# Performance work log

Measured on AMD Instinct MI355X. Metric: run time of the kernel, lower is better.

The kernel has to match this reference:

```python
import jax, jax.numpy as jnp
import numpy as np

MODEL = 2048
LATENT = 512
POS = 1024
NH = 16
HD = MODEL // NH        # 128
PHD = POS // NH         # 64
THETA = 50000.0


def _rope_tables(S, dim, base=THETA):
    inv_freq = 1.0 / (base ** (jnp.arange(0, dim, 2, dtype=jnp.float32) / dim))
    t = jnp.arange(S, dtype=jnp.float32)
    freqs = jnp.outer(t, inv_freq)                  # [S, dim/2]
    emb = jnp.concatenate([freqs, freqs], axis=-1)  # [S, dim]
    return jnp.cos(emb), jnp.sin(emb)


def _rotate_half(x):
    h = x.shape[-1] // 2
    return jnp.concatenate([-x[..., h:], x[..., :h]], axis=-1)


def _apply_rope(x, cos, sin):
    # x: [..., S, dim]; cos/sin: [S, dim]
    return x * cos + _rotate_half(x) * sin


def setup_inputs() -> dict:
    key = jax.random.key(0)
    ks = jax.random.split(key, 16)
    std = 0.02
    d = {
        'x':      jax.random.normal(ks[0], (2, 2048, MODEL), jnp.float32),
        'w_qkv':  jax.random.normal(ks[1], (MODEL, 3 * LATENT), jnp.float32) * std,
        'b_qkv':  jnp.zeros((3 * LATENT,), jnp.float32),
        'w_qup':  jax.random.normal(ks[2], (LATENT, MODEL), jnp.float32) * std,
        'b_qup':  jnp.zeros((MODEL,), jnp.float32),
        'w_kup':  jax.random.normal(ks[3], (LATENT, MODEL), jnp.float32) * std,
        'b_kup':  jnp.zeros((MODEL,), jnp.float32),
        'w_vup':  jax.random.normal(ks[4], (LATENT, MODEL), jnp.float32) * std,
        'b_vup':  jnp.zeros((MODEL,), jnp.float32),
        'w_qpos': jax.random.normal(ks[5], (LATENT, POS), jnp.float32) * std,
        'b_qpos': jnp.zeros((POS,), jnp.float32),
        'w_kpos': jax.random.normal(ks[6], (MODEL, PHD), jnp.float32) * std,
        'b_kpos': jnp.zeros((PHD,), jnp.float32),
        'w_o':    jax.random.normal(ks[7], (MODEL, MODEL), jnp.float32) * std,
        'b_o':    jnp.zeros((MODEL,), jnp.float32),
    }
    return d


def reference(x, w_qkv, b_qkv, w_qup, b_qup, w_kup, b_kup, w_vup, b_vup,
              w_qpos, b_qpos, w_kpos, b_kpos, w_o, b_o):
    B, S, _ = x.shape
    # fused down-projection into shared latent
    latent_qkv = x @ w_qkv + b_qkv                       # [B,S,3L]
    lq, lk, lv = jnp.split(latent_qkv, 3, axis=-1)       # each [B,S,L]

    cos, sin = _rope_tables(S, PHD)

    # decoupled positional key (shared across heads), RoPE on sub-slice
    pos_k = x @ w_kpos + b_kpos                          # [B,S,PHD]
    pos_k = _apply_rope(pos_k, cos, sin)

    # up-projections
    q = (lq @ w_qup + b_qup).reshape(B, S, NH, HD).transpose(0, 2, 1, 3)
    k = (lk @ w_kup + b_kup).reshape(B, S, NH, HD).transpose(0, 2, 1, 3)
    v = (lv @ w_vup + b_vup).reshape(B, S, NH, HD).transpose(0, 2, 1, 3)

    pos_q = (lq @ w_qpos + b_qpos).reshape(B, S, NH, PHD).transpose(0, 2, 1, 3)
    pos_q = _apply_rope(pos_q, cos, sin)                 # [B,NH,S,PHD]

    pos_kh = jnp.broadcast_to(pos_k[:, None], (B, NH, S, PHD))
    q = jnp.concatenate([q, pos_q], axis=-1)             # [B,NH,S,HD+PHD]
    k = jnp.concatenate([k, pos_kh], axis=-1)

    scale = 1.0 / jnp.sqrt(jnp.asarray(HD + PHD, x.dtype))
    scores = jnp.einsum('bhqd,bhkd->bhqk', q, k) * scale
    causal = jnp.tril(jnp.ones((S, S), bool))
    scores = jnp.where(causal, scores, jnp.finfo(scores.dtype).min)
    p = jax.nn.softmax(scores, axis=-1)
    attn = jnp.einsum('bhqk,bhkd->bhqd', p, v)           # [B,NH,S,HD]
    attn = attn.transpose(0, 2, 1, 3).reshape(B, S, MODEL)
    return attn @ w_o + b_o
```

## Files before the change

### kernel.cpp

```cpp
#include <hip/hip_runtime.h>
#include <cstdint>
#include <cstddef>

typedef __bf16 bf16x8 __attribute__((ext_vector_type(8)));
typedef float  f32x4  __attribute__((ext_vector_type(4)));
typedef unsigned short us8 __attribute__((ext_vector_type(8)));
typedef unsigned short us4 __attribute__((ext_vector_type(4)));

__device__ __forceinline__ unsigned short f2bf(float f) {
  union { float f; unsigned u; } v; v.f = f;
  unsigned r = v.u + 0x7FFFu + ((v.u >> 16) & 1u);
  return (unsigned short)(r >> 16);
}
__device__ __forceinline__ float b2f(unsigned short h) {
  union { unsigned u; float f; } v; v.u = ((unsigned)h) << 16;
  return v.f;
}
__device__ __forceinline__ f32x4 mfma16(bf16x8 a, bf16x8 b, f32x4 c) {
  return __builtin_amdgcn_mfma_f32_16x16x32_bf16(a, b, c, 0, 0, 0);
}
__device__ __forceinline__ void gl_lds16(const unsigned short* g, unsigned short* l) {
  __builtin_amdgcn_global_load_lds(
      (const __attribute__((address_space(1))) void*)g,
      (__attribute__((address_space(3))) void*)l, 16, 0, 0);
}

__global__ void prep_all_kernel(const float* __restrict__ b_qkv,
                                const float* __restrict__ b_kpos,
                                const float* __restrict__ b_qup,
                                const float* __restrict__ b_qpos,
                                float* __restrict__ bias1,
                                float* __restrict__ bias2q,
                                float* __restrict__ costab,
                                float* __restrict__ sintab,
                                unsigned short* __restrict__ wB1,
                                const float* __restrict__ w_qkv,
                                const float* __restrict__ w_kpos,
                                const float* __restrict__ w_qup,
                                const float* __restrict__ w_qpos,
                                const float* __restrict__ w_kup,
                                const float* __restrict__ w_vup,
                                const float* __restrict__ w_o,
                                unsigned short* __restrict__ wB2q,
                                unsigned short* __restrict__ wB2k,
                                unsigned short* __restrict__ wB2v,
                                unsigned short* __restrict__ wBo,
                                int* __restrict__ counters) {
  __shared__ float tile[32][33];
  int blk = blockIdx.x;
  if (blk < 512) {
    int i = blk * 256 + threadIdx.x;
    if (i < 65536) {
      int s = i >> 5, f = i & 31;
      float inv = powf(50000.0f, -(float)f / 32.0f);
      float a = (float)s * inv;
      costab[i] = cosf(a);
      sintab[i] = sinf(a);
    }
    if (i < 2048) bias1[i] = (i < 1536) ? b_qkv[i] : (i < 1600 ? b_kpos[i - 1536] : 0.0f);
    if (i < 3072) bias2q[i] = (i < 2048) ? b_qup[i] : b_qpos[i - 2048];
    for (int jj = 0; jj < 7; ++jj)
      wB1[(size_t)1600 * 2048 + (size_t)jj * 131072 + i] = 0;
    if (i < 64) counters[i] = 0;
    return;
  }
  const float* in;
  unsigned short* out;
  int ldin, ldo, nx, j;
  if (blk < 3584)      { j = blk - 512;  in = w_qkv;  ldin = 1536; out = wB1;                        ldo = 2048; nx = 48; }
  else if (blk < 3712) { j = blk - 3584; in = w_kpos; ldin = 64;   out = wB1 + (size_t)1536 * 2048;  ldo = 2048; nx = 2;  }
  else if (blk < 4736) { j = blk - 3712; in = w_qup;  ldin = 2048; out = wB2q;                       ldo = 512;  nx = 64; }
  else if (blk < 5248) { j = blk - 4736; in = w_qpos; ldin = 1024; out = wB2q + (size_t)2048 * 512;  ldo = 512;  nx = 32; }
  else if (blk < 6272) { j = blk - 5248; in = w_kup;  ldin = 2048; out = wB2k;                       ldo = 512;  nx = 64; }
  else if (blk < 7296) { j = blk - 6272; in = w_vup;  ldin = 2048; out = wB2v;                       ldo = 512;  nx = 64; }
  else                 { j = blk - 7296; in = w_o;    ldin = 2048; out = wBo;                        ldo = 2048; nx = 64; }
  int c0 = (j % nx) * 32, r0 = (j / nx) * 32;
  int tx = threadIdx.x & 31, ty = threadIdx.x >> 5;
  for (int jj = 0; jj < 4; ++jj)
    tile[ty + jj * 8][tx] = in[(size_t)(r0 + ty + jj * 8) * ldin + c0 + tx];
  __syncthreads();
  for (int jj = 0; jj < 4; ++jj)
    out[(size_t)(c0 + ty + jj * 8) * ldo + r0 + tx] = f2bf(tile[tx][ty + jj * 8]);
}

__device__ __forceinline__ void xcd_decode_n(int lbid, int nwg, int nx, int& bx, int& by) {
  int cpx = nwg >> 3;
  int wg = (lbid & 7) * cpx + (lbid >> 3);
  bx = wg % nx;
  by = wg / nx;
}
__device__ __forceinline__ void xcd_decode(int nx, int& bx, int& by) {
  xcd_decode_n(blockIdx.x, gridDim.x, nx, bx, by);
}

__device__ __forceinline__
void gemm_body(unsigned short* smem,
               const unsigned short* __restrict__ A, int lda,
               const unsigned short* __restrict__ Bt, int ldb,
               void* __restrict__ Cout, int ldc,
               const float* __restrict__ bias, int K,
               long brow, long bcol, int mode) {
  int tid = threadIdx.x;
  int wave = tid >> 6, lane = tid & 63;
  int g = lane >> 4, r = lane & 15;
  int wr = wave >> 1, wc = wave & 1;

  int srowl = lane >> 3;
  int sw = ((lane & 7) ^ (srowl & 7)) * 8;
  const unsigned short* Abase = A + (brow + wave * 32 + srowl) * (long)lda + sw;
  const unsigned short* Bbase = Bt + (bcol + wave * 32 + srowl) * (long)ldb + sw;

  f32x4 acc[4][4];
  for (int mi = 0; mi < 4; ++mi)
    for (int ni = 0; ni < 4; ++ni)
      acc[mi][ni] = f32x4{0.f, 0.f, 0.f, 0.f};

  auto stage = [&](int buf, int k0) {
    unsigned short* ab = smem + buf * 16384;
    unsigned short* bb = ab + 8192;
    for (int c = 0; c < 4; ++c) {
      gl_lds16(Abase + (size_t)c * 8 * lda + k0, ab + (wave * 32 + c * 8) * 64);
      gl_lds16(Bbase + (size_t)c * 8 * ldb + k0, bb + (wave * 32 + c * 8) * 64);
    }
  };

  int rx = (r & 7) << 4;
  int nt = K >> 6;

  stage(0, 0);
  for (int t = 0; t < nt; ++t) {
    if (t + 1 < nt) {
      stage((t + 1) & 1, (t + 1) << 6);
      asm volatile("s_waitcnt vmcnt(8)" ::: "memory");
    } else {
      asm volatile("s_waitcnt vmcnt(0)" ::: "memory");
    }
    __builtin_amdgcn_sched_barrier(0);
    __builtin_amdgcn_s_barrier();
    __builtin_amdgcn_sched_barrier(0);
    const char* Ab = (const char*)(smem + (t & 1) * 16384);
    const char* Bb = Ab + 16384;
    for (int kk = 0; kk < 2; ++kk) {
      bf16x8 af[4], bfv[4];
      for (int mi = 0; mi < 4; ++mi)
        af[mi] = *(const bf16x8*)(Ab + (size_t)(wr * 64 + mi * 16 + r) * 128 +
                                  ((kk * 64 + g * 16) ^ rx));
      for (int ni = 0; ni < 4; ++ni)
        bfv[ni] = *(const bf16x8*)(Bb + (size_t)(wc * 64 + ni * 16 + r) * 128 +
                                   ((kk * 64 + g * 16) ^ rx));
      for (int mi = 0; mi < 4; ++mi)
        for (int ni = 0; ni < 4; ++ni)
          acc[mi][ni] = mfma16(af[mi], bfv[ni], acc[mi][ni]);
    }
    __builtin_amdgcn_sched_barrier(0);
    __builtin_amdgcn_s_barrier();
  }

  if (mode == 2) {
    for (int mi = 0; mi < 4; ++mi)
      for (int ni = 0; ni < 4; ++ni) {
        int col = wc * 64 + ni * 16 + r;
        float bv = bias[bcol + col];
        int rowb = wr * 64 + mi * 16 + g * 4;
        for (int i = 0; i < 4; ++i)
          smem[col * 136 + rowb + i] = f2bf(acc[mi][ni][i] + bv);
      }
    __syncthreads();
    int col = tid >> 1, half = tid & 1;
    int bh = (int)(brow >> 11) * 16 + (int)(bcol >> 7);
    unsigned short* outp = (unsigned short*)Cout +
                           ((size_t)bh * 128 + col) * 2048 + (brow & 2047);
    for (int j = 0; j < 8; ++j) {
      int row0 = half * 64 + j * 8;
      *(us8*)(outp + row0) = *(const us8*)&smem[col * 136 + row0];
    }
    return;
  }

  for (int mi = 0; mi < 4; ++mi)
    for (int ni = 0; ni < 4; ++ni) {
      long col = bcol + wc * 64 + ni * 16 + r;
      float bv = bias ? bias[col] : 0.0f;
      long rowb = brow + wr * 64 + mi * 16 + g * 4;
      for (int i = 0; i < 4; ++i) {
        float v = acc[mi][ni][i] + bv;
        if (mode == 1)
          ((float*)Cout)[(rowb + i) * (long)ldc + col] = v;
        else
          ((unsigned short*)Cout)[(rowb + i) * (long)ldc + col] = f2bf(v);
      }
    }
}

template <int OUT_MODE>
__global__ __launch_bounds__(256, 2)
void gemm_bt_kernel(const unsigned short* __restrict__ A, int lda,
                    const unsigned short* __restrict__ Bt, int ldb,
                    void* __restrict__ Cout, int ldc,
                    const float* __restrict__ bias, int K, int nx) {
  __shared__ unsigned short smem[32768];
  int bx, by;
  xcd_decode(nx, bx, by);
  gemm_body(smem, A, lda, Bt, ldb, Cout, ldc, bias, K,
            (long)by * 128, (long)bx * 128, OUT_MODE);
}

__global__ __launch_bounds__(256, 2)
void gemm_up3_kernel(const unsigned short* __restrict__ latext,
                     const unsigned short* __restrict__ wB2q,
                     const unsigned short* __restrict__ wB2k,
                     const unsigned short* __restrict__ wB2v,
                     unsigned short* __restrict__ tmp_q,
                     unsigned short* __restrict__ tmp_k,
                     unsigned short* __restrict__ vTbuf,
                     const float* __restrict__ bias2q,
                     const float* __restrict__ b_kup,
                     const float* __restrict__ b_vup) {
  __shared__ unsigned short smem[32768];
  int bid = blockIdx.x;
  const unsigned short* A;
  const unsigned short* Bt;
  void* C;
  const float* bias;
  int ldc, nx, mode, lbid, nwg;
  if (bid < 768)       { lbid = bid;        nwg = 768; nx = 24; A = latext;        Bt = wB2q; C = tmp_q; ldc = 3072; bias = bias2q; mode = 0; }
  else if (bid < 1280) { lbid = bid - 768;  nwg = 512; nx = 16; A = latext + 512;  Bt = wB2k; C = tmp_k; ldc = 2048; bias = b_kup;  mode = 0; }
  else                 { lbid = bid - 1280; nwg = 512; nx = 16; A = latext + 1024; Bt = wB2v; C = vTbuf; ldc = 2048; bias = b_vup;  mode = 2; }
  int bx, by;
  xcd_decode_n(lbid, nwg, nx, bx, by);
  gemm_body(smem, A, 2048, Bt, 512, C, ldc, bias, 512,
            (long)by * 128, (long)bx * 128, mode);
}

__global__ __launch_bounds__(256, 2)
void gemm_a32_kernel(const float* __restrict__ A, int lda,
                     const unsigned short* __restrict__ Bt, int ldb,
                     unsigned short* __restrict__ Cout, int ldc,
                     const float* __restrict__ bias, int K, int nx) {
  __shared__ unsigned short smem[32768];
  int tid = threadIdx.x;
  int wave = tid >> 6, lane = tid & 63;
  int g = lane >> 4, r = lane & 15;
  int wr = wave >> 1, wc = wave & 1;
  int bx, by;
  xcd_decode(nx, bx, by);
  long brow = (long)by * 128, bcol = (long)bx * 128;

  int f4c = tid & 15, row0 = tid >> 4;
  int ablk = f4c >> 1, asub = (f4c & 1) * 8;
  const float4* Ag = (const float4*)(A + (brow + row0) * (size_t)lda) + f4c;

  int srowl = lane >> 3;
  int sw = ((lane & 7) ^ (srowl & 7)) * 8;
  const unsigned short* Bbase = Bt + (bcol + wave * 32 + srowl) * (long)ldb + sw;

  f32x4 acc[4][4];
  for (int mi = 0; mi < 4; ++mi)
    for (int ni = 0; ni < 4; ++ni)
      acc[mi][ni] = f32x4{0.f, 0.f, 0.f, 0.f};

  auto stage_b = [&](int buf, int k0) {
    unsigned short* bb = smem + 16384 + buf * 8192;
    for (int c = 0; c < 4; ++c)
      gl_lds16(Bbase + (size_t)c * 8 * ldb + k0, bb + (wave * 32 + c * 8) * 64);
  };

  int rx = (r & 7) << 4;
  int nt = K >> 6;

  float4 areg[8];
#pragma unroll
  for (int s = 0; s < 8; ++s) areg[s] = Ag[(size_t)s * 8192];
  stage_b(0, 0);

  for (int t = 0; t < nt; ++t) {
    char* alds = (char*)(smem + (t & 1) * 8192);
#pragma unroll
    for (int s = 0; s < 8; ++s) {
      us4 hv;
      hv[0] = f2bf(areg[s].x); hv[1] = f2bf(areg[s].y);
      hv[2] = f2bf(areg[s].z); hv[3] = f2bf(areg[s].w);
      int row = row0 + s * 16;
      *(us4*)(alds + row * 128 + ((ablk ^ (row & 7)) << 4) + asub) = hv;
    }
    asm volatile("s_waitcnt vmcnt(0)" ::: "memory");
    asm volatile("s_waitcnt lgkmcnt(0)" ::: "memory");
    __builtin_amdgcn_sched_barrier(0);
    __builtin_amdgcn_s_barrier();
    __builtin_amdgcn_sched_barrier(0);
    if (t + 1 < nt) {
      int k1 = (t + 1) << 6;
#pragma unroll
      for (int s = 0; s < 8; ++s) areg[s] = Ag[(size_t)s * 8192 + (k1 >> 2)];
      stage_b((t + 1) & 1, k1);
    }
    const char* Ab = (const char*)(smem + (t & 1) * 8192);
    const char* Bb = (const char*)(smem + 16384 + (t & 1) * 8192);
    for (int kk = 0; kk < 2; ++kk) {
      bf16x8 af[4], bfv[4];
      for (int mi = 0; mi < 4; ++mi)
        af[mi] = *(const bf16x8*)(Ab + (size_t)(wr * 64 + mi * 16 + r) * 128 +
                                  ((kk * 64 + g * 16) ^ rx));
      for (int ni = 0; ni < 4; ++ni)
        bfv[ni] = *(const bf16x8*)(Bb + (size_t)(wc * 64 + ni * 16 + r) * 128 +
                                   ((kk * 64 + g * 16) ^ rx));
      for (int mi = 0; mi < 4; ++mi)
        for (int ni = 0; ni < 4; ++ni)
          acc[mi][ni] = mfma16(af[mi], bfv[ni], acc[mi][ni]);
    }
    __builtin_amdgcn_sched_barrier(0);
    __builtin_amdgcn_s_barrier();
  }

  for (int mi = 0; mi < 4; ++mi)
    for (int ni = 0; ni < 4; ++ni) {
      long col = bcol + wc * 64 + ni * 16 + r;
      float bv = bias[col];
      long rowb = brow + wr * 64 + mi * 16 + g * 4;
      for (int i = 0; i < 4; ++i)
        Cout[(rowb + i) * (long)ldc + col] = f2bf(acc[mi][ni][i] + bv);
    }
}

__global__ void rope_kernel(const unsigned short* __restrict__ tmp_q,
                            const unsigned short* __restrict__ latext,
                            const float* __restrict__ costab,
                            const float* __restrict__ sintab,
                            unsigned short* __restrict__ posqr,
                            unsigned short* __restrict__ poskr) {
  int idx = blockIdx.x * 256 + threadIdx.x;
  const unsigned short* src;
  unsigned short* dst;
  int s, dp0;
  if (idx < 524288) {
    int rowA = idx >> 7, rem = idx & 127;
    int h = rem >> 3;
    dp0 = (rem & 7) * 8;
    s = rowA & 2047;
    src = tmp_q + (size_t)rowA * 3072 + 2048 + h * 64;
    dst = posqr + (size_t)rowA * 1024 + h * 64 + dp0;
  } else if (idx < 557056) {
    int j = idx - 524288;
    int rowA = j >> 3;
    dp0 = (j & 7) * 8;
    s = rowA & 2047;
    src = latext + (size_t)rowA * 2048 + 1536;
    dst = poskr + (size_t)rowA * 64 + dp0;
  } else {
    return;
  }
  us8 x1 = *(const us8*)(src + dp0);
  us8 x2 = *(const us8*)(src + (dp0 ^ 32));
  int f0 = dp0 & 31;
  const float* cp = costab + s * 32 + f0;
  const float* sp = sintab + s * 32 + f0;
  bool low = dp0 < 32;
  us8 o;
  for (int e = 0; e < 8; ++e) {
    float a = b2f(x1[e]), b = b2f(x2[e]);
    float v = low ? (a * cp[e] - b * sp[e]) : (a * cp[e] + b * sp[e]);
    o[e] = f2bf(v);
  }
  *(us8*)dst = o;
}

__device__ __forceinline__ void task_decode(int t, int& qt, int& seg, int& bh) {
  if (t < 1024) {
    qt = 31 - (t >> 7); int rem = t & 127; seg = rem >> 5; bh = rem & 31;
  } else if (t < 1792) {
    int t2 = t - 1024; int qi = t2 / 96; int rem = t2 - qi * 96;
    qt = 23 - qi; seg = rem >> 5; bh = rem & 31;
  } else if (t < 2304) {
    int t3 = t - 1792; qt = 15 - (t3 >> 6); int rem = t3 & 63; seg = rem >> 5; bh = rem & 31;
  } else {
    int t4 = t - 2304; qt = 7 - (t4 >> 5); seg = 0; bh = t4 & 31;
  }
}
__device__ __forceinline__ int task_slot(int qt, int seg, int bh) {
  if (qt >= 24) return (31 - qt) * 128 + seg * 32 + bh;
  if (qt >= 16) return 1024 + (23 - qt) * 96 + seg * 32 + bh;
  return 1792 + (15 - qt) * 64 + seg * 32 + bh;
}

__global__ __launch_bounds__(256, 2)
void flash_kernel(const unsigned short* __restrict__ tmp_q,
                  const unsigned short* __restrict__ tmp_k,
                  const unsigned short* __restrict__ posqr,
                  const unsigned short* __restrict__ poskr,
                  const unsigned short* __restrict__ vT,
                  unsigned short* __restrict__ ob,
                  unsigned short* __restrict__ Opart,
                  float* __restrict__ mlbuf,
                  int* __restrict__ counter) {
  const int S = 2048;
  int tid = threadIdx.x, wave = tid >> 6, lane = tid & 63;
  int g = lane >> 4, r = lane & 15;
  const float sl2 = 1.44269504f / 13.8564064605510183f;
  const float DEFER = 96.0f;

  __shared__ unsigned short Klds[32 * 192];
  __shared__ unsigned short Vlds[64 * 64];
  __shared__ unsigned short Plds[4][16][40];
  __shared__ int s_tile;
  char* Kb = (char*)Klds;
  char* Vb = (char*)Vlds;
  int rx7 = (r & 7) << 4;

  us8 onesu;
  for (int e = 0; e < 8; ++e) onesu[e] = 0x3F80;
  bf16x8 ones = *(const bf16x8*)&onesu;

  int kn_row[2], kn_seg[2];
  for (int j = 0; j < 2; ++j) {
    int slot = j * 256 + tid;
    kn_row[j] = slot >> 4;
    kn_seg[j] = slot & 15;
  }
  int kr_row = tid >> 3, kr_seg = tid & 7;
  int v_row[2], v_seg[2];
  for (int j = 0; j < 2; ++j) {
    int slot = j * 256 + tid;
    v_row[j] = slot >> 2;
    v_seg[j] = slot & 3;
  }

  for (;;) {
    if (tid == 0) s_tile = atomicAdd(counter, 1);
    __syncthreads();
    int t = s_tile;
    if (t >= 2560) return;
    int qt, seg, bh;
    task_decode(t, qt, seg, bh);
    int b = bh >> 4, h = bh & 15;
    int qbase = qt * 64;
    int cbeg = seg * 16;
    int cend = min(cbeg + 16, 2 * (qt + 1));
    size_t rb = (size_t)b * 2048;

    const unsigned short* kpn = tmp_k + rb * 2048 + h * 128;
    const unsigned short* kpr = poskr + rb * 64;
    const unsigned short* vp = vT + (size_t)bh * 128 * S;

    bf16x8 qf[6];
    {
      size_t qrowA = rb + qbase + wave * 16 + r;
      const unsigned short* qn = tmp_q + qrowA * 3072 + h * 128 + g * 8;
      for (int c = 0; c < 4; ++c) qf[c] = *(const bf16x8*)(qn + c * 32);
      const unsigned short* qr_ = posqr + qrowA * 1024 + h * 64 + g * 8;
      qf[4] = *(const bf16x8*)(qr_);
      qf[5] = *(const bf16x8*)(qr_ + 32);
    }

    f32x4 acc[8];
    for (int d = 0; d < 8; ++d) acc[d] = f32x4{0.f, 0.f, 0.f, 0.f};
    f32x4 lacc = {0.f, 0.f, 0.f, 0.f};
    float m_r[4];
    for (int i = 0; i < 4; ++i) m_r[i] = -3.0e38f;

    us8 kreg[2], krope, vreg[2];
    {
      int kv0 = cbeg * 32;
      for (int j = 0; j < 2; ++j)
        kreg[j] = *(const us8*)(kpn + (size_t)(kv0 + kn_row[j]) * 2048 + kn_seg[j] * 8);
      krope = *(const us8*)(kpr + (size_t)(kv0 + kr_row) * 64 + kr_seg * 8);
      for (int j = 0; j < 2; ++j)
        vreg[j] = *(const us8*)(vp + (size_t)v_row[j] * S + kv0 + v_seg[j] * 8);
    }

    for (int ch = cbeg; ch < cend; ++ch) {
      for (int j = 0; j < 2; ++j)
        *(us8*)(Kb + (size_t)kn_row[j] * 384 +
                ((kn_seg[j] ^ (kn_row[j] & 7)) << 4)) = kreg[j];
      *(us8*)(Kb + (size_t)kr_row * 384 +
              (((16 + kr_seg) ^ (kr_row & 7)) << 4)) = krope;
      for (int j = 0; j < 2; ++j) {
        int d = v_row[j];
        *(us8*)(Vb + (size_t)(d & 63) * 128 +
                ((((d >> 6) * 4 + v_seg[j]) ^ (d & 7)) << 4)) = vreg[j];
      }
      asm volatile("s_waitcnt lgkmcnt(0)" ::: "memory");
      __builtin_amdgcn_sched_barrier(0);
      __builtin_amdgcn_s_barrier();
      __builtin_amdgcn_sched_barrier(0);
      if (ch + 1 < cend) {
        int kv1 = (ch + 1) * 32;
        for (int j = 0; j < 2; ++j)
          kreg[j] = *(const us8*)(kpn + (size_t)(kv1 + kn_row[j]) * 2048 + kn_seg[j] * 8);
        krope = *(const us8*)(kpr + (size_t)(kv1 + kr_row) * 64 + kr_seg * 8);
        for (int j = 0; j < 2; ++j)
          vreg[j] = *(const us8*)(vp + (size_t)v_row[j] * S + kv1 + v_seg[j] * 8);
      }
      int kv0 = ch * 32;

      f32x4 sc0 = {0.f, 0.f, 0.f, 0.f}, sc1 = {0.f, 0.f, 0.f, 0.f};
      __builtin_amdgcn_s_setprio(1);
      for (int c = 0; c < 6; ++c) {
        bf16x8 kf0 = *(const bf16x8*)(Kb + (size_t)r * 384 + (((c * 4 + g) << 4) ^ rx7));
        sc0 = mfma16(qf[c], kf0, sc0);
      }
      for (int c = 0; c < 6; ++c) {
        bf16x8 kf1 = *(const bf16x8*)(Kb + (size_t)(16 + r) * 384 + (((c * 4 + g) << 4) ^ rx7));
        sc1 = mfma16(qf[c], kf1, sc1);
      }
      __builtin_amdgcn_s_setprio(0);

      int qi_min = qbase + wave * 16;
      if (kv0 + 31 > qi_min) {
        int kj0 = kv0 + r, kj1 = kv0 + 16 + r;
        int qi0 = qi_min + g * 4;
        for (int i = 0; i < 4; ++i) {
          if (kj0 > qi0 + i) sc0[i] = -1e30f;
          if (kj1 > qi0 + i) sc1[i] = -1e30f;
        }
      }

      float tl[4];
      bool ok = true;
      for (int i = 0; i < 4; ++i) {
        tl[i] = fmaxf(sc0[i], sc1[i]);
        ok = ok && (tl[i] - m_r[i] <= DEFER);
      }
      if (!__all(ok)) {
        for (int i = 0; i < 4; ++i) {
          float tm = tl[i];
          for (int off = 1; off < 16; off <<= 1) tm = fmaxf(tm, __shfl_xor(tm, off, 64));
          float mnew = fmaxf(m_r[i], tm);
          float corr = exp2f((m_r[i] - mnew) * sl2);
          lacc[i] *= corr;
          for (int d = 0; d < 8; ++d) acc[d][i] *= corr;
          m_r[i] = mnew;
        }
      }
      float p0[4], p1[4];
      for (int i = 0; i < 4; ++i) {
        p0[i] = exp2f((sc0[i] - m_r[i]) * sl2);
        p1[i] = exp2f((sc1[i] - m_r[i]) * sl2);
      }

      for (int i = 0; i < 4; ++i) {
        Plds[wave][g * 4 + i][r] = f2bf(p0[i]);
        Plds[wave][g * 4 + i][16 + r] = f2bf(p1[i]);
      }
      bf16x8 pa = *(const bf16x8*)&Plds[wave][r][g * 8];
      __builtin_amdgcn_s_setprio(1);
      lacc = mfma16(pa, ones, lacc);
      for (int dt = 0; dt < 8; ++dt) {
        bf16x8 vf = *(const bf16x8*)(Vb + (size_t)((dt & 3) * 16 + r) * 128 +
                                     ((((dt >> 2) * 4 + g) << 4) ^ rx7));
        acc[dt] = mfma16(pa, vf, acc[dt]);
      }
      __builtin_amdgcn_s_setprio(0);
      __builtin_amdgcn_sched_barrier(0);
      __builtin_amdgcn_s_barrier();
    }

    if (qt <= 7) {
      for (int i = 0; i < 4; ++i) {
        float inv = 1.0f / lacc[i];
        int row = qbase + wave * 16 + g * 4 + i;
        size_t base = (rb + row) * 2048 + h * 128;
        for (int dt = 0; dt < 8; ++dt)
          ob[base + dt * 16 + r] = f2bf(acc[dt][i] * inv);
      }
    } else {
      unsigned short* op = Opart + (size_t)t * 8192;
      for (int i = 0; i < 4; ++i) {
        int row = wave * 16 + g * 4 + i;
        for (int dt = 0; dt < 8; ++dt)
          op[row * 128 + dt * 16 + r] = f2bf(acc[dt][i]);
        if (r == 0) {
          mlbuf[(size_t)t * 128 + row * 2]     = m_r[i];
          mlbuf[(size_t)t * 128 + row * 2 + 1] = lacc[i];
        }
      }
    }
  }
}

__global__ void merge_kernel(const unsigned short* __restrict__ Opart,
                             const float* __restrict__ mlbuf,
                             unsigned short* __restrict__ ob) {
  int qt = 8 + (blockIdx.x >> 5), bh = blockIdx.x & 31;
  int b = bh >> 4, h = bh & 15;
  int tid = threadIdx.x;
  int row = tid >> 2, c0 = (tid & 3) * 32;
  const float sl2 = 1.44269504f / 13.8564064605510183f;
  int ns = (qt >= 24) ? 4 : (qt >= 16 ? 3 : 2);

  size_t slot[4];
  float m[4], l[4], w[4];
  float M = -3.0e38f;
#pragma unroll
  for (int j = 0; j < 4; ++j) {
    if (j < ns) {
      slot[j] = task_slot(qt, j, bh);
      m[j] = mlbuf[slot[j] * 128 + row * 2];
      l[j] = mlbuf[slot[j] * 128 + row * 2 + 1];
      M = fmaxf(M, m[j]);
    }
  }
  float L = 0.f;
#pragma unroll
  for (int j = 0; j < 4; ++j)
    if (j < ns) { w[j] = exp2f((m[j] - M) * sl2); L += w[j] * l[j]; }
  float invL = 1.f / L;
#pragma unroll
  for (int j = 0; j < 4; ++j) if (j < ns) w[j] *= invL;

  float o[32];
#pragma unroll
  for (int e = 0; e < 32; ++e) o[e] = 0.f;
#pragma unroll
  for (int j = 0; j < 4; ++j) {
    if (j < ns) {
      const unsigned short* pp = Opart + slot[j] * 8192 + row * 128 + c0;
      for (int blk = 0; blk < 4; ++blk) {
        us8 v = *(const us8*)(pp + blk * 8);
        for (int e = 0; e < 8; ++e) o[blk * 8 + e] += w[j] * b2f(v[e]);
      }
    }
  }
  size_t obase = ((size_t)b * 2048 + qt * 64 + row) * 2048 + h * 128 + c0;
  for (int blk = 0; blk < 4; ++blk) {
    us8 st;
    for (int e = 0; e < 8; ++e) st[e] = f2bf(o[blk * 8 + e]);
    *(us8*)(ob + obase + blk * 8) = st;
  }
}

extern "C" void kernel_launch(void* const* d_in, const int* in_sizes, int n_in,
                              void* d_out, int out_size, void* d_ws, size_t ws_size,
                              hipStream_t stream) {
  const float* x      = (const float*)d_in[0];
  const float* w_qkv  = (const float*)d_in[1];
  const float* b_qkv  = (const float*)d_in[2];
  const float* w_qup  = (const float*)d_in[3];
  const float* b_qup  = (const float*)d_in[4];
  const float* w_kup  = (const float*)d_in[5];
  const float* b_kup  = (const float*)d_in[6];
  const float* w_vup  = (const float*)d_in[7];
  const float* b_vup  = (const float*)d_in[8];
  const float* w_qpos = (const float*)d_in[9];
  const float* b_qpos = (const float*)d_in[10];
  const float* w_kpos = (const float*)d_in[11];
  const float* b_kpos = (const float*)d_in[12];
  const float* w_o    = (const float*)d_in[13];
  const float* b_o    = (const float*)d_in[14];
  (void)in_sizes; (void)n_in; (void)out_size; (void)ws_size;

  char* ws = (char*)d_ws;
  size_t off = 0;
  auto alloc = [&](size_t bytes) -> char* {
    char* p = ws + off;
    off += (bytes + 255) & ~(size_t)255;
    return p;
  };

  unsigned short* wB1    = (unsigned short*)alloc(8388608);
  unsigned short* wB2q   = (unsigned short*)alloc(3145728);
  unsigned short* wB2k   = (unsigned short*)alloc(2097152);
  unsigned short* wB2v   = (unsigned short*)alloc(2097152);
  unsigned short* wBo    = (unsigned short*)alloc(8388608);
  float*          bias1  = (float*)alloc(2048 * 4);
  float*          bias2q = (float*)alloc(3072 * 4);
  float*          costab = (float*)alloc(262144);
  float*          sintab = (float*)alloc(262144);
  unsigned short* latext = (unsigned short*)alloc(16777216);
  unsigned short* tmp_q  = (unsigned short*)alloc(25165824);
  unsigned short* tmp_k  = (unsigned short*)alloc(16777216);
  unsigned short* vTbuf  = (unsigned short*)alloc(16777216);
  unsigned short* posqr  = (unsigned short*)alloc(8388608);
  unsigned short* poskr  = (unsigned short*)alloc(524288);
  unsigned short* Opart  = (unsigned short*)alloc(41943040);
  float*          mlbuf  = (float*)alloc(1310720);
  int*            counter= (int*)alloc(256);
  unsigned short* attnb  = (unsigned short*)alloc(16777216);

  prep_all_kernel<<<11392, 256, 0, stream>>>(b_qkv, b_kpos, b_qup, b_qpos,
                                             bias1, bias2q, costab, sintab, wB1,
                                             w_qkv, w_kpos, w_qup, w_qpos, w_kup,
                                             w_vup, w_o, wB2q, wB2k, wB2v, wBo,
                                             counter);
  gemm_a32_kernel<<<512, 256, 0, stream>>>(x, 2048, wB1, 2048,
                                           latext, 2048, bias1, 2048, 16);
  gemm_up3_kernel<<<1792, 256, 0, stream>>>(latext, wB2q, wB2k, wB2v,
                                            tmp_q, tmp_k, vTbuf,
                                            bias2q, b_kup, b_vup);
  rope_kernel<<<2176, 256, 0, stream>>>(tmp_q, latext, costab, sintab, posqr, poskr);
  flash_kernel<<<1280, 256, 0, stream>>>(tmp_q, tmp_k, posqr, poskr, vTbuf,
                                         attnb, Opart, mlbuf, counter);
  merge_kernel<<<768, 256, 0, stream>>>(Opart, mlbuf, attnb);
  gemm_bt_kernel<1><<<512, 256, 0, stream>>>(attnb, 2048, wBo, 2048,
                                             d_out, 2048, b_o, 2048, 16);
}
```

Measured before the change: 270.2 us.

## Fuse RoPE into GEMM epilogues and drop the standalone rope kernel

Applies the rotary embedding directly in the epilogues of the latent down-projection (positional key columns) and the query up-projection (positional query columns), writing posqr/poskr directly. The separate rope kernel, its launch and the bf16 round-trip through tmp_q/latext are removed, and tmp_q shrinks to 2048 columns. The down-projection grid is trimmed from 16 to 13 column tiles, since the padding tiles past the positional-key block are no longer needed. The trade-off is that epilogue stores become scalar bf16 writes with extra cos/sin table loads.

```diff
diff --git a/kernel.cpp b/kernel.cpp
--- a/kernel.cpp
+++ b/kernel.cpp
@@ -99,7 +99,8 @@
                const unsigned short* __restrict__ Bt, int ldb,
                void* __restrict__ Cout, int ldc,
                const float* __restrict__ bias, int K,
-               long brow, long bcol, int mode) {
+               long brow, long bcol, int mode,
+               const float* __restrict__ ct, const float* __restrict__ st) {
   int tid = threadIdx.x;
   int wave = tid >> 6, lane = tid & 63;
   int g = lane >> 4, r = lane & 15;
@@ -177,6 +178,31 @@
     return;
   }
 
+  if (mode == 3) {
+    float bv[4];
+    for (int ni = 0; ni < 4; ++ni)
+      bv[ni] = bias[bcol + wc * 64 + ni * 16 + r];
+    unsigned short* outp = (unsigned short*)Cout;
+    long cbase = bcol - 2048 + wc * 64;
+    for (int mi = 0; mi < 4; ++mi)
+      for (int i = 0; i < 4; ++i) {
+        long row = brow + wr * 64 + mi * 16 + g * 4 + i;
+        int s = (int)(row & 2047);
+        float c0 = ct[s * 32 + r],      sn0 = st[s * 32 + r];
+        float c1 = ct[s * 32 + 16 + r], sn1 = st[s * 32 + 16 + r];
+        float v0 = acc[mi][0][i] + bv[0];
+        float v1 = acc[mi][1][i] + bv[1];
+        float v2 = acc[mi][2][i] + bv[2];
+        float v3 = acc[mi][3][i] + bv[3];
+        size_t base = (size_t)row * 1024 + cbase;
+        outp[base + r]      = f2bf(v0 * c0 - v2 * sn0);
+        outp[base + 16 + r] = f2bf(v1 * c1 - v3 * sn1);
+        outp[base + 32 + r] = f2bf(v2 * c0 + v0 * sn0);
+        outp[base + 48 + r] = f2bf(v3 * c1 + v1 * sn1);
+      }
+    return;
+  }
+
   for (int mi = 0; mi < 4; ++mi)
     for (int ni = 0; ni < 4; ++ni) {
       long col = bcol + wc * 64 + ni * 16 + r;
@@ -202,7 +228,7 @@
   int bx, by;
   xcd_decode(nx, bx, by);
   gemm_body(smem, A, lda, Bt, ldb, Cout, ldc, bias, K,
-            (long)by * 128, (long)bx * 128, OUT_MODE);
+            (long)by * 128, (long)bx * 128, OUT_MODE, nullptr, nullptr);
 }
 
 __global__ __launch_bounds__(256, 2)
@@ -213,9 +239,12 @@
                      unsigned short* __restrict__ tmp_q,
                      unsigned short* __restrict__ tmp_k,
                      unsigned short* __restrict__ vTbuf,
+                     unsigned short* __restrict__ posqr,
                      const float* __restrict__ bias2q,
                      const float* __restrict__ b_kup,
-                     const float* __restrict__ b_vup) {
+                     const float* __restrict__ b_vup,
+                     const float* __restrict__ costab,
+                     const float* __restrict__ sintab) {
   __shared__ unsigned short smem[32768];
   int bid = blockIdx.x;
   const unsigned short* A;
@@ -223,20 +252,27 @@
   void* C;
   const float* bias;
   int ldc, nx, mode, lbid, nwg;
-  if (bid < 768)       { lbid = bid;        nwg = 768; nx = 24; A = latext;        Bt = wB2q; C = tmp_q; ldc = 3072; bias = bias2q; mode = 0; }
-  else if (bid < 1280) { lbid = bid - 768;  nwg = 512; nx = 16; A = latext + 512;  Bt = wB2k; C = tmp_k; ldc = 2048; bias = b_kup;  mode = 0; }
-  else                 { lbid = bid - 1280; nwg = 512; nx = 16; A = latext + 1024; Bt = wB2v; C = vTbuf; ldc = 2048; bias = b_vup;  mode = 2; }
+  if (bid < 768)       { lbid = bid;        nwg = 768; nx = 24; A = latext;        Bt = wB2q; bias = bias2q; ldc = 2048; }
+  else if (bid < 1280) { lbid = bid - 768;  nwg = 512; nx = 16; A = latext + 512;  Bt = wB2k; C = tmp_k; ldc = 2048; bias = b_kup; mode = 0; }
+  else                 { lbid = bid - 1280; nwg = 512; nx = 16; A = latext + 1024; Bt = wB2v; C = vTbuf; ldc = 2048; bias = b_vup; mode = 2; }
   int bx, by;
   xcd_decode_n(lbid, nwg, nx, bx, by);
+  if (bid < 768) {
+    if (bx >= 16) { C = posqr; mode = 3; }
+    else          { C = tmp_q; mode = 0; }
+  }
   gemm_body(smem, A, 2048, Bt, 512, C, ldc, bias, 512,
-            (long)by * 128, (long)bx * 128, mode);
+            (long)by * 128, (long)bx * 128, mode, costab, sintab);
 }
 
 __global__ __launch_bounds__(256, 2)
 void gemm_a32_kernel(const float* __restrict__ A, int lda,
                      const unsigned short* __restrict__ Bt, int ldb,
                      unsigned short* __restrict__ Cout, int ldc,
-                     const float* __restrict__ bias, int K, int nx) {
+                     const float* __restrict__ bias, int K, int nx,
+                     unsigned short* __restrict__ poskr,
+                     const float* __restrict__ costab,
+                     const float* __restrict__ sintab) {
   __shared__ unsigned short smem[32768];
   int tid = threadIdx.x;
   int wave = tid >> 6, lane = tid & 63;
@@ -312,6 +348,31 @@
     __builtin_amdgcn_s_barrier();
   }
 
+  if (bx == 12) {
+    if (wc == 0) {
+      float bv[4];
+      for (int ni = 0; ni < 4; ++ni)
+        bv[ni] = bias[1536 + ni * 16 + r];
+      for (int mi = 0; mi < 4; ++mi)
+        for (int i = 0; i < 4; ++i) {
+          long row = brow + wr * 64 + mi * 16 + g * 4 + i;
+          int s = (int)(row & 2047);
+          float c0 = costab[s * 32 + r],      sn0 = sintab[s * 32 + r];
+          float c1 = costab[s * 32 + 16 + r], sn1 = sintab[s * 32 + 16 + r];
+          float v0 = acc[mi][0][i] + bv[0];
+          float v1 = acc[mi][1][i] + bv[1];
+          float v2 = acc[mi][2][i] + bv[2];
+          float v3 = acc[mi][3][i] + bv[3];
+          size_t base = (size_t)row * 64;
+          poskr[base + r]      = f2bf(v0 * c0 - v2 * sn0);
+          poskr[base + 16 + r] = f2bf(v1 * c1 - v3 * sn1);
+          poskr[base + 32 + r] = f2bf(v2 * c0 + v0 * sn0);
+          poskr[base + 48 + r] = f2bf(v3 * c1 + v1 * sn1);
+        }
+    }
+    return;
+  }
+
   for (int mi = 0; mi < 4; ++mi)
     for (int ni = 0; ni < 4; ++ni) {
       long col = bcol + wc * 64 + ni * 16 + r;
@@ -320,48 +381,6 @@
       for (int i = 0; i < 4; ++i)
         Cout[(rowb + i) * (long)ldc + col] = f2bf(acc[mi][ni][i] + bv);
     }
-}
-
-__global__ void rope_kernel(const unsigned short* __restrict__ tmp_q,
-                            const unsigned short* __restrict__ latext,
-                            const float* __restrict__ costab,
-                            const float* __restrict__ sintab,
-                            unsigned short* __restrict__ posqr,
-                            unsigned short* __restrict__ poskr) {
-  int idx = blockIdx.x * 256 + threadIdx.x;
-  const unsigned short* src;
-  unsigned short* dst;
-  int s, dp0;
-  if (idx < 524288) {
-    int rowA = idx >> 7, rem = idx & 127;
-    int h = rem >> 3;
-    dp0 = (rem & 7) * 8;
-    s = rowA & 2047;
-    src = tmp_q + (size_t)rowA * 3072 + 2048 + h * 64;
-    dst = posqr + (size_t)rowA * 1024 + h * 64 + dp0;
-  } else if (idx < 557056) {
-    int j = idx - 524288;
-    int rowA = j >> 3;
-    dp0 = (j & 7) * 8;
-    s = rowA & 2047;
-    src = latext + (size_t)rowA * 2048 + 1536;
-    dst = poskr + (size_t)rowA * 64 + dp0;
-  } else {
-    return;
-  }
-  us8 x1 = *(const us8*)(src + dp0);
-  us8 x2 = *(const us8*)(src + (dp0 ^ 32));
-  int f0 = dp0 & 31;
-  const float* cp = costab + s * 32 + f0;
-  const float* sp = sintab + s * 32 + f0;
-  bool low = dp0 < 32;
-  us8 o;
-  for (int e = 0; e < 8; ++e) {
-    float a = b2f(x1[e]), b = b2f(x2[e]);
-    float v = low ? (a * cp[e] - b * sp[e]) : (a * cp[e] + b * sp[e]);
-    o[e] = f2bf(v);
-  }
-  *(us8*)dst = o;
 }
 
 __device__ __forceinline__ void task_decode(int t, int& qt, int& seg, int& bh) {
@@ -444,7 +463,7 @@
     bf16x8 qf[6];
     {
       size_t qrowA = rb + qbase + wave * 16 + r;
-      const unsigned short* qn = tmp_q + qrowA * 3072 + h * 128 + g * 8;
+      const unsigned short* qn = tmp_q + qrowA * 2048 + h * 128 + g * 8;
       for (int c = 0; c < 4; ++c) qf[c] = *(const bf16x8*)(qn + c * 32);
       const unsigned short* qr_ = posqr + qrowA * 1024 + h * 64 + g * 8;
       qf[4] = *(const bf16x8*)(qr_);
@@ -666,7 +685,7 @@
   float*          costab = (float*)alloc(262144);
   float*          sintab = (float*)alloc(262144);
   unsigned short* latext = (unsigned short*)alloc(16777216);
-  unsigned short* tmp_q  = (unsigned short*)alloc(25165824);
+  unsigned short* tmp_q  = (unsigned short*)alloc(16777216);
   unsigned short* tmp_k  = (unsigned short*)alloc(16777216);
   unsigned short* vTbuf  = (unsigned short*)alloc(16777216);
   unsigned short* posqr  = (unsigned short*)alloc(8388608);
@@ -681,12 +700,12 @@
                                              w_qkv, w_kpos, w_qup, w_qpos, w_kup,
                                              w_vup, w_o, wB2q, wB2k, wB2v, wBo,
                                              counter);
-  gemm_a32_kernel<<<512, 256, 0, stream>>>(x, 2048, wB1, 2048,
-                                           latext, 2048, bias1, 2048, 16);
+  gemm_a32_kernel<<<416, 256, 0, stream>>>(x, 2048, wB1, 2048,
+                                           latext, 2048, bias1, 2048, 13,
+                                           poskr, costab, sintab);
   gemm_up3_kernel<<<1792, 256, 0, stream>>>(latext, wB2q, wB2k, wB2v,
-                                            tmp_q, tmp_k, vTbuf,
-                                            bias2q, b_kup, b_vup);
-  rope_kernel<<<2176, 256, 0, stream>>>(tmp_q, latext, costab, sintab, posqr, poskr);
+                                            tmp_q, tmp_k, vTbuf, posqr,
+                                            bias2q, b_kup, b_vup, costab, sintab);
   flash_kernel<<<1280, 256, 0, stream>>>(tmp_q, tmp_k, posqr, poskr, vTbuf,
                                          attnb, Opart, mlbuf, counter);
   merge_kernel<<<768, 256, 0, stream>>>(Opart, mlbuf, attnb);
```

Result: no change. 265.0 us (-1.9%).
